# Kernel optimization log

Hardware: AMD Instinct MI355X
Metric: run time of the kernel (lower is better)

## Reference

```python
import jax, jax.numpy as jnp
import numpy as np

T, B, E, H = 2048, 2, 1024, 16
S = E // H


def setup_inputs() -> dict:
    key = jax.random.key(0)
    ks = jax.random.split(key, 7)
    sc = 1.0 / np.sqrt(S)
    return {
        "x": jax.random.normal(ks[0], (T, B, E), dtype=jnp.float32),
        "Wq": jax.random.normal(ks[1], (H, S, S), dtype=jnp.float32) * sc,
        "Wk": jax.random.normal(ks[2], (H, S, S), dtype=jnp.float32) * sc,
        "Wv": jax.random.normal(ks[3], (H, S, S), dtype=jnp.float32) * sc,
        "Er": jax.random.normal(ks[4], (S, T), dtype=jnp.float32),
        "Wr": jax.random.normal(ks[5], (E, E), dtype=jnp.float32) * (1.0 / np.sqrt(E)),
        "br": jax.random.normal(ks[6], (E,), dtype=jnp.float32) * 0.01,
    }


def reference(x, Wq, Wk, Wv, Er, Wr, br):
    # x: [t, b, e] -> [b, t, h, s]
    t, b, e = x.shape
    h = Wq.shape[0]
    s = e // h
    xh = jnp.transpose(x, (1, 0, 2)).reshape(b, t, h, s)
    # per-head no-bias linears (nn.Linear: y = x @ W.T), stacked over heads
    q = jnp.einsum('bths,hds->bhtd', xh, Wq)  # [b,h,t,s]
    k = jnp.einsum('bths,hds->bhtd', xh, Wk)
    v = jnp.einsum('bths,hds->bhtd', xh, Wv)
    # relative bias uses UNSCALED queries (computed before the 1/e^(1/4) scaling)
    srel = jnp.einsum('bhtd,dr->bhtr', q, Er)  # [b,h,t,t] since r == t
    scale = e ** 0.25
    scores = jnp.einsum('bhtd,bhrd->bhtr', q / scale, k / scale) + srel
    causal = jnp.triu(jnp.ones((t, t), dtype=bool), 1)
    scores = jnp.where(causal[None, None], jnp.float32(-1e9), scores)
    probs = jax.nn.softmax(scores, axis=-1)  # dropout is identity in eval
    out = jnp.einsum('bhtr,bhrd->bhtd', probs, v)  # [b,h,t,s]
    # torch.cat(heads, dim=2) == move head axis next to s
    out = jnp.transpose(out, (0, 2, 1, 3)).reshape(b, t, h * s)  # [b,t,e]
    # faithful to source quirk: transpose(1,2).contiguous().view(b,t,e)
    out = jnp.swapaxes(out, 1, 2).reshape(b, t, h * s)
    return out @ Wr.T + br
```

## Files before the change

### kernel.cpp

```cpp
#include <hip/hip_runtime.h>
#include <hip/hip_bf16.h>
#include <cstdio>

#define T_DIM 2048
#define B_DIM 2
#define E_DIM 1024
#define H_DIM 16
#define S_DIM 64
#define LOG2E 1.44269504088896340736f

typedef __attribute__((ext_vector_type(4))) float f32x4;
typedef __attribute__((ext_vector_type(16))) float f32x16;
typedef __attribute__((ext_vector_type(8))) short bf16x8;
typedef __attribute__((ext_vector_type(8))) unsigned short u16x8;
typedef __attribute__((ext_vector_type(4))) unsigned short u16x4;

#define MFMA32(a,b,c) __builtin_amdgcn_mfma_f32_32x32x16_bf16((a),(b),(c),0,0,0)

__device__ __forceinline__ unsigned short f2bf(float f) {
    union { __hip_bfloat16 h; unsigned short u; } c;
    c.h = __float2bfloat16(f);
    return c.u;
}
__device__ __forceinline__ void gload16(const void* g, void* l) {
    __builtin_amdgcn_global_load_lds(
        (const __attribute__((address_space(1))) unsigned int*)g,
        (__attribute__((address_space(3))) unsigned int*)l, 16, 0, 0);
}
__device__ __forceinline__ f32x16 zero16() {
    f32x16 v;
#pragma unroll
    for (int i = 0; i < 16; ++i) v[i] = 0.f;
    return v;
}

__global__ __launch_bounds__(256) void prep_w(
    const float* __restrict__ Wq, const float* __restrict__ Wk,
    const float* __restrict__ Wv, const float* __restrict__ Wr,
    unsigned short* __restrict__ whb, unsigned short* __restrict__ wrb)
{
    int bid = blockIdx.x;
    if (bid < 192) {
        int i = bid * 256 + threadIdx.x;
        const float* src = (i < 16384) ? Wq : ((i < 32768) ? Wk : Wv);
        float4 v = reinterpret_cast<const float4*>(src)[i & 16383];
        u16x4 o;
        o[0] = f2bf(v.x); o[1] = f2bf(v.y); o[2] = f2bf(v.z); o[3] = f2bf(v.w);
        *reinterpret_cast<u16x4*>(whb + (size_t)i * 4) = o;
    } else {
        int i = (bid - 192) * 256 + threadIdx.x;
        float4 v = reinterpret_cast<const float4*>(Wr)[i];
        u16x4 o;
        o[0] = f2bf(v.x); o[1] = f2bf(v.y); o[2] = f2bf(v.z); o[3] = f2bf(v.w);
        *reinterpret_cast<u16x4*>(wrb + (size_t)i * 4) = o;
    }
}

__global__ __launch_bounds__(64) void qkv_mfma(
    const float* __restrict__ x, const unsigned short* __restrict__ wb,
    const float* __restrict__ Er,
    unsigned short* __restrict__ qb_g, unsigned short* __restrict__ kh_g,
    unsigned short* __restrict__ vT_g)
{
    int bid = blockIdx.x;
    int tt = bid & 63;
    int h  = (bid >> 6) & 15;
    int b  = bid >> 10;
    int bh = b * H_DIM + h;
    int t0 = tt * 32;
    int lane = threadIdx.x;
    int l31 = lane & 31, hs = lane >> 5;

    bf16x8 xb[4];
    const float* xrow = x + (size_t)(t0 + l31) * (B_DIM * E_DIM) + (size_t)b * E_DIM + h * 64;
#pragma unroll
    for (int ks = 0; ks < 4; ++ks) {
        float vv[8];
        *reinterpret_cast<float4*>(&vv[0]) = *reinterpret_cast<const float4*>(xrow + ks * 16 + hs * 8);
        *reinterpret_cast<float4*>(&vv[4]) = *reinterpret_cast<const float4*>(xrow + ks * 16 + hs * 8 + 4);
        unsigned short hh[8];
#pragma unroll
        for (int j = 0; j < 8; ++j) hh[j] = f2bf(vv[j]);
        xb[ks] = *reinterpret_cast<bf16x8*>(hh);
    }

    size_t rowbase = (size_t)bh * T_DIM * 64;
#pragma unroll 1
    for (int dg = 0; dg < 2; ++dg) {
        f32x16 aq = zero16(), ak = zero16(), av = zero16();
        size_t wofs = (size_t)h * 4096 + (size_t)(dg * 32 + l31) * 64 + hs * 8;
#pragma unroll
        for (int ks = 0; ks < 4; ++ks) {
            bf16x8 qw = *reinterpret_cast<const bf16x8*>(wb + wofs + ks * 16);
            bf16x8 kw = *reinterpret_cast<const bf16x8*>(wb + 65536 + wofs + ks * 16);
            bf16x8 vw = *reinterpret_cast<const bf16x8*>(wb + 131072 + wofs + ks * 16);
            aq = MFMA32(xb[ks], qw, aq);
            ak = MFMA32(xb[ks], kw, ak);
            av = MFMA32(vw, xb[ks], av);
        }
#pragma unroll
        for (int r = 0; r < 16; ++r) {
            int rowp = (r & 3) + 8 * (r >> 2) + 4 * hs;
            int t = t0 + rowp;
            int d = dg * 32 + l31;
            size_t ro = rowbase + (size_t)t * 64 + d;
            qb_g[ro] = f2bf(aq[r]);
            float kv = (ak[r] * 0.03125f + Er[(size_t)d * T_DIM + t]) * LOG2E;
            kh_g[ro] = f2bf(kv);
            vT_g[((size_t)bh * 64 + dg * 32 + rowp) * T_DIM + t0 + l31] = f2bf(av[r]);
        }
    }
}

__global__ __launch_bounds__(256, 4) void attn_mfma32(
    const unsigned short* __restrict__ qb_g, const unsigned short* __restrict__ kh_g,
    const unsigned short* __restrict__ vT_g, unsigned short* __restrict__ attT)
{
    __shared__ __align__(16) unsigned char smem[32768];
    float* OT  = (float*)smem;
    float* MRG = (float*)smem;
    float* ML  = (float*)(smem + 16384);

    int bid = blockIdx.x;
    int bh = bid & 31;
    int u = bid >> 5;
    int j = u & 7, quad = u >> 3;
    int qt = (quad == 0) ? (31 - j) : (quad == 1) ? j
           : (quad == 2) ? (23 - j) : (8 + j);

    int tid = threadIdx.x;
    int w = tid >> 6;
    int half = w >> 1;
    int wq = w & 1;
    int lane = tid & 63;
    int l31 = lane & 31, hs = lane >> 5;
    int srow = lane >> 3, scol = lane & 7;
    int lsw = (l31 & 7) ^ (((l31 >> 3) & 3) << 1);
    int q_lo = qt * 64 + wq * 32;
    size_t base = (size_t)bh * T_DIM * 64;

    bf16x8 qB[4];
    {
        size_t qoff = base + (size_t)(q_lo + l31) * 64 + hs * 8;
#pragma unroll
        for (int st = 0; st < 4; ++st)
            qB[st] = *reinterpret_cast<const bf16x8*>(qb_g + qoff + st * 16);
    }

    f32x16 oacc0 = zero16(), oacc1 = zero16();
    float lsum = 0.f;

    unsigned char* KH = smem + half * 16384;
    unsigned char* VT = KH + 8192;

    auto qk = [&](int kt) -> f32x16 {
        int krow = kt * 32 + l31;
        f32x16 s = zero16();
        __builtin_amdgcn_s_setprio(1);
#pragma unroll
        for (int st = 0; st < 4; ++st) {
            int slot = (st * 2 + hs) ^ lsw;
            bf16x8 kf = *reinterpret_cast<const bf16x8*>(KH + krow * 128 + slot * 16);
            s = MFMA32(kf, qB[st], s);
        }
        __builtin_amdgcn_s_setprio(0);
        return s;
    };

    auto smpv = [&](f32x16& s, int kt, bool diag) {
        if (diag) {
#pragma unroll
            for (int r = 0; r < 16; ++r) {
                int rowp = (r & 3) + 8 * (r >> 2) + 4 * hs;
                if (rowp > l31) s[r] = -1e30f;
            }
        }
        float p[16], psum = 0.f;
#pragma unroll
        for (int r = 0; r < 16; ++r) {
            p[r] = __builtin_amdgcn_exp2f(s[r]);
            psum += p[r];
        }
        lsum += psum + __shfl_xor(psum, 32);
        unsigned int wp[8];
#pragma unroll
        for (int q2 = 0; q2 < 2; ++q2) {
            int o = q2 * 8, d2 = q2 * 4;
            asm("v_cvt_pk_bf16_f32 %0, %1, %2" : "=v"(wp[d2+0]) : "v"(p[o+0]), "v"(p[o+1]));
            asm("v_cvt_pk_bf16_f32 %0, %1, %2" : "=v"(wp[d2+1]) : "v"(p[o+2]), "v"(p[o+3]));
            asm("v_cvt_pk_bf16_f32 %0, %1, %2" : "=v"(wp[d2+2]) : "v"(p[o+4]), "v"(p[o+5]));
            asm("v_cvt_pk_bf16_f32 %0, %1, %2" : "=v"(wp[d2+3]) : "v"(p[o+6]), "v"(p[o+7]));
            asm("v_permlane32_swap_b32 %0, %1" : "+v"(wp[d2+0]), "+v"(wp[d2+2]));
            asm("v_permlane32_swap_b32 %0, %1" : "+v"(wp[d2+1]), "+v"(wp[d2+3]));
        }
        union { unsigned int u[4]; bf16x8 v; } pa0, pa1;
        pa0.u[0] = wp[0]; pa0.u[1] = wp[1]; pa0.u[2] = wp[2]; pa0.u[3] = wp[3];
        pa1.u[0] = wp[4]; pa1.u[1] = wp[5]; pa1.u[2] = wp[6]; pa1.u[3] = wp[7];
        __builtin_amdgcn_s_setprio(1);
#pragma unroll
        for (int ph = 0; ph < 2; ++ph) {
            const bf16x8 pv = ph ? pa1.v : pa0.v;
#pragma unroll
            for (int dt = 0; dt < 2; ++dt) {
                int c = kt * 4 + ph * 2 + hs;
                int slot = c ^ lsw;
                bf16x8 vb = *reinterpret_cast<const bf16x8*>(VT + (dt * 32 + l31) * 128 + slot * 16);
                if (dt == 0) oacc0 = MFMA32(vb, pv, oacc0);
                else         oacc1 = MFMA32(vb, pv, oacc1);
            }
        }
        __builtin_amdgcn_s_setprio(0);
    };

    int ntiles = qt + 1;
    int nst = (ntiles + 1) >> 1;

    for (int i = 0; i < nst; ++i) {
        int k0 = (2 * i + half) * 64;
        bool valid = k0 < ntiles * 64;
        __syncthreads();
        if (valid) {
#pragma unroll
            for (int ci = 0; ci < 4; ++ci) {
                int chunk = wq * 4 + ci;
                int row = chunk * 8 + srow;
                int cd = scol ^ srow ^ ((ci & 3) << 1);
                gload16(kh_g + base + (size_t)(k0 + row) * 64 + cd * 8,
                        KH + chunk * 1024 + lane * 16);
            }
#pragma unroll
            for (int ci = 0; ci < 4; ++ci) {
                int chunk = wq * 4 + ci;
                int d = chunk * 8 + srow;
                int cd = scol ^ srow ^ ((ci & 3) << 1);
                gload16(vT_g + base + (size_t)d * T_DIM + k0 + cd * 8,
                        VT + chunk * 1024 + lane * 16);
            }
        }
        __syncthreads();
        if (valid) {
            bool two = (k0 + 32 <= q_lo);
            f32x16 s0 = qk(0);
            if (two) {
                f32x16 s1 = qk(1);
                smpv(s0, 0, false);
                smpv(s1, 1, k0 + 32 == q_lo);
            } else {
                smpv(s0, 0, k0 == q_lo);
            }
        }
    }

    __syncthreads();
    if (half == 1) {
#pragma unroll
        for (int r = 0; r < 16; ++r) {
            MRG[(wq * 32 + r) * 64 + lane]      = oacc0[r];
            MRG[(wq * 32 + 16 + r) * 64 + lane] = oacc1[r];
        }
        if (hs == 0) ML[wq * 32 + l31] = lsum;
    }
    __syncthreads();
    float inv = 0.f;
    if (half == 0) {
        lsum += ML[wq * 32 + l31];
        inv = 1.f / lsum;
#pragma unroll
        for (int r = 0; r < 16; ++r) {
            oacc0[r] += MRG[(wq * 32 + r) * 64 + lane];
            oacc1[r] += MRG[(wq * 32 + 16 + r) * 64 + lane];
        }
    }
    __syncthreads();

    if (half == 0) {
#pragma unroll
        for (int r = 0; r < 16; ++r) {
            int rowp = (r & 3) + 8 * (r >> 2) + 4 * hs;
            OT[(rowp)      * 68 + wq * 32 + l31] = oacc0[r] * inv;
            OT[(32 + rowp) * 68 + wq * 32 + l31] = oacc1[r] * inv;
        }
    }
    __syncthreads();
    {
        int d = tid >> 2, qb = tid & 3;
        unsigned short tmp[16];
#pragma unroll
        for (int i = 0; i < 4; ++i) {
            f32x4 v = *reinterpret_cast<const f32x4*>(&OT[d * 68 + qb * 16 + i * 4]);
            tmp[i*4+0] = f2bf(v[0]); tmp[i*4+1] = f2bf(v[1]);
            tmp[i*4+2] = f2bf(v[2]); tmp[i*4+3] = f2bf(v[3]);
        }
        unsigned short* dst = attT + ((size_t)bh * 64 + d) * T_DIM + qt * 64 + qb * 16;
        *reinterpret_cast<u16x8*>(dst)     = *reinterpret_cast<u16x8*>(&tmp[0]);
        *reinterpret_cast<u16x8*>(dst + 8) = *reinterpret_cast<u16x8*>(&tmp[8]);
    }
}

__global__ __launch_bounds__(256) void final_gemm_mfma(
    const unsigned short* __restrict__ A, const unsigned short* __restrict__ Bw,
    const float* __restrict__ br, float* __restrict__ out)
{
    __shared__ __align__(16) unsigned char gsm[49152];
    int nt = blockIdx.x;
    int mt = blockIdx.y;
    int tid = threadIdx.x;
    int w = tid >> 6;
    int lane = tid & 63;
    int l31 = lane & 31, hs = lane >> 5;
    int srow = lane >> 3, scol = lane & 7;
    int lsw = (l31 & 7) ^ (((l31 >> 3) & 3) << 1);

    auto stage = [&](int bs, int kt) {
        unsigned char* As = gsm + bs * 24576;
        unsigned char* Bs = As + 16384;
#pragma unroll
        for (int i = 0; i < 4; ++i) {
            int row = i * 32 + w * 8 + srow;
            int cd = scol ^ srow ^ (((row >> 3) & 3) << 1);
            gload16(A + (size_t)(mt * 128 + row) * 1024 + kt * 64 + cd * 8,
                    As + i * 4096 + w * 1024 + lane * 16);
        }
#pragma unroll
        for (int i = 0; i < 2; ++i) {
            int row = i * 32 + w * 8 + srow;
            int cd = scol ^ srow ^ (((row >> 3) & 3) << 1);
            gload16(Bw + (size_t)(nt * 64 + row) * 1024 + kt * 64 + cd * 8,
                    Bs + i * 4096 + w * 1024 + lane * 16);
        }
    };

    f32x16 oa0 = zero16(), oa1 = zero16();
    stage(0, 0);
    __syncthreads();
    for (int kt = 0; kt < 16; ++kt) {
        if (kt < 15) stage((kt + 1) & 1, kt + 1);
        const unsigned char* As = gsm + (kt & 1) * 24576;
        const unsigned char* Bs = As + 16384;
        int arow = w * 32 + l31;
        int asw = (arow & 7) ^ (((arow >> 3) & 3) << 1);
        __builtin_amdgcn_s_setprio(1);
#pragma unroll
        for (int st = 0; st < 4; ++st) {
            int c = st * 2 + hs;
            bf16x8 af = *reinterpret_cast<const bf16x8*>(As + arow * 128 + ((c ^ asw) * 16));
            {
                bf16x8 bf0 = *reinterpret_cast<const bf16x8*>(Bs + l31 * 128 + ((c ^ lsw) * 16));
                oa0 = MFMA32(af, bf0, oa0);
            }
            {
                int brow = 32 + l31;
                bf16x8 bf1 = *reinterpret_cast<const bf16x8*>(Bs + brow * 128 + ((c ^ lsw) * 16));
                oa1 = MFMA32(af, bf1, oa1);
            }
        }
        __builtin_amdgcn_s_setprio(0);
        __syncthreads();
    }

#pragma unroll
    for (int ng = 0; ng < 2; ++ng) {
        int col = nt * 64 + ng * 32 + l31;
        float bias = br[col];
        const f32x16& oa = ng ? oa1 : oa0;
#pragma unroll
        for (int r = 0; r < 16; ++r) {
            int rowp = (r & 3) + 8 * (r >> 2) + 4 * hs;
            int row = mt * 128 + w * 32 + rowp;
            out[(size_t)row * 1024 + col] = oa[r] + bias;
        }
    }
}

extern "C" void kernel_launch(void* const* d_in, const int* in_sizes, int n_in,
                              void* d_out, int out_size, void* d_ws, size_t ws_size,
                              hipStream_t stream) {
    const float* x  = (const float*)d_in[0];
    const float* Wq = (const float*)d_in[1];
    const float* Wk = (const float*)d_in[2];
    const float* Wv = (const float*)d_in[3];
    const float* Er = (const float*)d_in[4];
    const float* Wr = (const float*)d_in[5];
    const float* br = (const float*)d_in[6];
    float* out = (float*)d_out;

    const size_t nQ = (size_t)B_DIM * H_DIM * T_DIM * S_DIM;
    char* p = (char*)d_ws;
    unsigned short* qb = (unsigned short*)p;   p += nQ * 2;
    unsigned short* kh = (unsigned short*)p;   p += nQ * 2;
    unsigned short* vT = (unsigned short*)p;   p += nQ * 2;
    unsigned short* attT = (unsigned short*)p; p += nQ * 2;
    unsigned short* wrb = (unsigned short*)p;  p += (size_t)E_DIM * E_DIM * 2;
    unsigned short* whb = (unsigned short*)p;  p += (size_t)3 * 65536 * 2;
    size_t need = (size_t)(p - (char*)d_ws);
    if (ws_size < need) {
        fprintf(stderr, "WS TOO SMALL: have %zu need %zu\n", ws_size, need);
        return;
    }

    prep_w<<<1216, 256, 0, stream>>>(Wq, Wk, Wv, Wr, whb, wrb);
    qkv_mfma<<<2048, 64, 0, stream>>>(x, whb, Er, qb, kh, vT);
    attn_mfma32<<<1024, 256, 0, stream>>>(qb, kh, vT, attT);
    final_gemm_mfma<<<dim3(16, 32), 256, 0, stream>>>(attT, wrb, br, out);
}
```

Before: 73.00 us.

## Double-buffer 32-row K/V tiles to overlap global loads with attention compute

```diff
diff --git a/kernel.cpp b/kernel.cpp
--- a/kernel.cpp
+++ b/kernel.cpp
@@ -135,6 +135,7 @@
     int lane = tid & 63;
     int l31 = lane & 31, hs = lane >> 5;
     int srow = lane >> 3, scol = lane & 7;
+    int vrow = lane >> 2, vcol = lane & 3;
     int lsw = (l31 & 7) ^ (((l31 >> 3) & 3) << 1);
     int q_lo = qt * 64 + wq * 32;
     size_t base = (size_t)bh * T_DIM * 64;
@@ -150,25 +151,40 @@
     f32x16 oacc0 = zero16(), oacc1 = zero16();
     float lsum = 0.f;
 
-    unsigned char* KH = smem + half * 16384;
-    unsigned char* VT = KH + 8192;
-
-    auto qk = [&](int kt) -> f32x16 {
-        int krow = kt * 32 + l31;
+    unsigned char* hbase = smem + half * 16384;
+
+    auto stage = [&](int bs, int k0) {
+        unsigned char* KH = hbase + bs * 8192;
+        unsigned char* VT = KH + 4096;
+#pragma unroll
+        for (int ci = 0; ci < 2; ++ci) {
+            int row = ci * 16 + wq * 8 + srow;
+            int swz = (row & 7) ^ (((row >> 3) & 3) << 1);
+            gload16(kh_g + base + (size_t)(k0 + row) * 64 + (scol ^ swz) * 8,
+                    KH + ci * 2048 + wq * 1024 + lane * 16);
+        }
+#pragma unroll
+        for (int ci = 0; ci < 2; ++ci) {
+            int d = ci * 32 + wq * 16 + vrow;
+            int swz = (d >> 1) & 3;
+            gload16(vT_g + base + (size_t)d * T_DIM + k0 + ((vcol ^ swz) & 3) * 8,
+                    VT + ci * 2048 + wq * 1024 + lane * 16);
+        }
+    };
+
+    auto compute = [&](int bs, int k0) {
+        const unsigned char* KH = hbase + bs * 8192;
+        const unsigned char* VT = KH + 4096;
         f32x16 s = zero16();
         __builtin_amdgcn_s_setprio(1);
 #pragma unroll
         for (int st = 0; st < 4; ++st) {
             int slot = (st * 2 + hs) ^ lsw;
-            bf16x8 kf = *reinterpret_cast<const bf16x8*>(KH + krow * 128 + slot * 16);
+            bf16x8 kf = *reinterpret_cast<const bf16x8*>(KH + l31 * 128 + slot * 16);
             s = MFMA32(kf, qB[st], s);
         }
         __builtin_amdgcn_s_setprio(0);
-        return s;
-    };
-
-    auto smpv = [&](f32x16& s, int kt, bool diag) {
-        if (diag) {
+        if (k0 == q_lo) {
 #pragma unroll
             for (int r = 0; r < 16; ++r) {
                 int rowp = (r & 3) + 8 * (r >> 2) + 4 * hs;
@@ -202,9 +218,9 @@
             const bf16x8 pv = ph ? pa1.v : pa0.v;
 #pragma unroll
             for (int dt = 0; dt < 2; ++dt) {
-                int c = kt * 4 + ph * 2 + hs;
-                int slot = c ^ lsw;
-                bf16x8 vb = *reinterpret_cast<const bf16x8*>(VT + (dt * 32 + l31) * 128 + slot * 16);
+                int d = dt * 32 + l31;
+                int slot = ((ph * 2 + hs) ^ ((d >> 1) & 3)) & 3;
+                bf16x8 vb = *reinterpret_cast<const bf16x8*>(VT + d * 64 + slot * 16);
                 if (dt == 0) oacc0 = MFMA32(vb, pv, oacc0);
                 else         oacc1 = MFMA32(vb, pv, oacc1);
             }
@@ -212,46 +228,15 @@
         __builtin_amdgcn_s_setprio(0);
     };
 
-    int ntiles = qt + 1;
-    int nst = (ntiles + 1) >> 1;
-
-    for (int i = 0; i < nst; ++i) {
-        int k0 = (2 * i + half) * 64;
-        bool valid = k0 < ntiles * 64;
+    stage(0, half * 32);
+    __syncthreads();
+    for (int i = 0; i <= qt; ++i) {
+        int k0 = (2 * i + half) * 32;
+        if (i < qt) stage((i + 1) & 1, (2 * (i + 1) + half) * 32);
+        if (k0 <= q_lo) compute(i & 1, k0);
         __syncthreads();
-        if (valid) {
-#pragma unroll
-            for (int ci = 0; ci < 4; ++ci) {
-                int chunk = wq * 4 + ci;
-                int row = chunk * 8 + srow;
-                int cd = scol ^ srow ^ ((ci & 3) << 1);
-                gload16(kh_g + base + (size_t)(k0 + row) * 64 + cd * 8,
-                        KH + chunk * 1024 + lane * 16);
-            }
-#pragma unroll
-            for (int ci = 0; ci < 4; ++ci) {
-                int chunk = wq * 4 + ci;
-                int d = chunk * 8 + srow;
-                int cd = scol ^ srow ^ ((ci & 3) << 1);
-                gload16(vT_g + base + (size_t)d * T_DIM + k0 + cd * 8,
-                        VT + chunk * 1024 + lane * 16);
-            }
-        }
-        __syncthreads();
-        if (valid) {
-            bool two = (k0 + 32 <= q_lo);
-            f32x16 s0 = qk(0);
-            if (two) {
-                f32x16 s1 = qk(1);
-                smpv(s0, 0, false);
-                smpv(s1, 1, k0 + 32 == q_lo);
-            } else {
-                smpv(s0, 0, k0 == q_lo);
-            }
-        }
-    }
-
-    __syncthreads();
+    }
+
     if (half == 1) {
 #pragma unroll
         for (int r = 0; r < 16; ++r) {
```

Result: no change. 72.17 us, median of 3 (-1.1%).
